# Performance work log

Hardware: AMD Instinct MI355X
Metric: run time of the kernel (lower is better)

The kernel has to match this reference:

```python
import jax, jax.numpy as jnp
import numpy as np


def _bitrev_indices(N):
    # bit-reversal permutation, vectorized in numpy (static, N known at trace time)
    bits = int(np.log2(N))
    idx = np.arange(N, dtype=np.int64)
    rev = np.zeros(N, dtype=np.int64)
    for _ in range(bits):
        rev = (rev << 1) | (idx & 1)
        idx >>= 1
    return jnp.asarray(rev)


def setup_inputs() -> dict:
    key = jax.random.key(0)
    k1, k2 = jax.random.split(key)
    B, N = 2048, 4096
    return {
        "x_re": jax.random.normal(k1, (B, N), dtype=jnp.float32),
        "x_im": jax.random.normal(k2, (B, N), dtype=jnp.float32),
    }


def reference(x_re, x_im):
    # Radix-2 decimation-in-time Cooley-Tukey FFT, faithful to PythonFFT.forward
    N = x_re.shape[-1]
    batch = x_re.shape[:-1]
    num_stages = int(np.log2(N))

    # twiddle table W_N^k = exp(-2*pi*i*k/N) (matches compute_twiddle_table)
    k = jnp.arange(N, dtype=jnp.float32)
    angles = (-2.0 * np.pi) * k / N
    W_re_tab = jnp.cos(angles)
    W_im_tab = jnp.sin(angles)

    br = _bitrev_indices(N)
    y_re = x_re[..., br]
    y_im = x_im[..., br]

    # loop over log2(N) stages (small fixed loop); each stage is fully vectorized
    for stage in range(num_stages):
        stride = 1 << stage
        group = stride << 1
        # twiddle index for butterfly position j in a group: j * (N // group) % N
        tw_idx = (jnp.arange(stride) * (N // group)) % N
        w_re = W_re_tab[tw_idx]  # [stride]
        w_im = W_im_tab[tw_idx]  # [stride]

        yr = y_re.reshape(*batch, N // group, 2, stride)
        yi = y_im.reshape(*batch, N // group, 2, stride)
        a_re, b_re = yr[..., 0, :], yr[..., 1, :]
        a_im, b_im = yi[..., 0, :], yi[..., 1, :]

        wb_re = w_re * b_re - w_im * b_im
        wb_im = w_re * b_im + w_im * b_re

        y_re = jnp.stack([a_re + wb_re, a_re - wb_re], axis=-2).reshape(*batch, N)
        y_im = jnp.stack([a_im + wb_im, a_im - wb_im], axis=-2).reshape(*batch, N)

    return (y_re, y_im)
```

## Files before the change

### kernel.cpp

```cpp
#include <hip/hip_runtime.h>
#include <math.h>

#define FFT_N   4096
#define LOGN    12
#define THREADS 512
#define NEG2PI_N (-1.5339807878856412e-3f)

__device__ __forceinline__ int SW2(int i) { return i ^ ((i >> 5) & 31); }

__device__ __forceinline__ float2 cmul(float2 a, float2 b) {
    return make_float2(a.x * b.x - a.y * b.y, a.x * b.y + a.y * b.x);
}

__device__ __forceinline__ void bfly(float2& a, float2& b, float2 w) {
    float tr = w.x * b.x - w.y * b.y;
    float ti = w.x * b.y + w.y * b.x;
    b = make_float2(a.x - tr, a.y - ti);
    a = make_float2(a.x + tr, a.y + ti);
}

template<int ST, bool WRITE>
__device__ __forceinline__ void radix8_stage(float2* __restrict__ sd, int t, float2* v)
{
    const int s    = 1 << ST;
    const int lo   = t & (s - 1);
    const int base = ((t >> ST) << (ST + 3)) | lo;

    int addr[8];
    #pragma unroll
    for (int k = 0; k < 8; ++k) addr[k] = SW2(base + k * s);
    #pragma unroll
    for (int k = 0; k < 8; ++k) v[k] = sd[addr[k]];

    float ang = (float)(lo << (9 - ST)) * NEG2PI_N;
    float sn, cs;
    __sincosf(ang, &sn, &cs);
    const float2 wc0 = make_float2(cs, sn);
    const float2 wb0 = cmul(wc0, wc0);
    const float2 wa  = cmul(wb0, wb0);

    bfly(v[0], v[1], wa); bfly(v[2], v[3], wa);
    bfly(v[4], v[5], wa); bfly(v[6], v[7], wa);

    const float2 wb1 = make_float2(wb0.y, -wb0.x);
    bfly(v[0], v[2], wb0); bfly(v[1], v[3], wb1);
    bfly(v[4], v[6], wb0); bfly(v[5], v[7], wb1);

    const float RH = 0.70710678118654752f;
    const float2 wc1 = cmul(wc0, make_float2(RH, -RH));
    const float2 wc2 = make_float2(wc0.y, -wc0.x);
    const float2 wc3 = cmul(wc0, make_float2(-RH, -RH));
    bfly(v[0], v[4], wc0); bfly(v[1], v[5], wc1);
    bfly(v[2], v[6], wc2); bfly(v[3], v[7], wc3);

    if (WRITE) {
        #pragma unroll
        for (int k = 0; k < 8; ++k) sd[addr[k]] = v[k];
    }
}

__global__ __launch_bounds__(THREADS)
void fft4096_r8(const float* __restrict__ xre, const float* __restrict__ xim,
                float* __restrict__ yre, float* __restrict__ yim)
{
    __shared__ float2 sd[FFT_N];
    const int t = threadIdx.x;
    const size_t off = (size_t)blockIdx.x * FFT_N;

    const float4* xr4 = (const float4*)(xre + off);
    const float4* xi4 = (const float4*)(xim + off);
    float4 r0 = xr4[t];
    float4 r1 = xr4[t + THREADS];
    float4 m0 = xi4[t];
    float4 m1 = xi4[t + THREADS];

    const int rb = (int)(__brev((unsigned)t) >> 23) << 1;
    sd[SW2(rb + (0 << 10))]     = make_float2(r0.x, m0.x);
    sd[SW2(rb + (2 << 10))]     = make_float2(r0.y, m0.y);
    sd[SW2(rb + (1 << 10))]     = make_float2(r0.z, m0.z);
    sd[SW2(rb + (3 << 10))]     = make_float2(r0.w, m0.w);
    sd[SW2(rb + 1)]             = make_float2(r1.x, m1.x);
    sd[SW2(rb + 1 + (2 << 10))] = make_float2(r1.y, m1.y);
    sd[SW2(rb + 1 + (1 << 10))] = make_float2(r1.z, m1.z);
    sd[SW2(rb + 1 + (3 << 10))] = make_float2(r1.w, m1.w);
    __syncthreads();

    float2 v[8];
    radix8_stage<0, true>(sd, t, v);  __syncthreads();
    radix8_stage<3, true>(sd, t, v);  __syncthreads();
    radix8_stage<6, true>(sd, t, v);  __syncthreads();
    radix8_stage<9, false>(sd, t, v);

    float* yr = yre + off;
    float* yi = yim + off;
    #pragma unroll
    for (int k = 0; k < 8; ++k) {
        yr[t + (k << 9)] = v[k].x;
        yi[t + (k << 9)] = v[k].y;
    }
}

extern "C" void kernel_launch(void* const* d_in, const int* in_sizes, int n_in,
                              void* d_out, int out_size, void* d_ws, size_t ws_size,
                              hipStream_t stream) {
    const float* xre = (const float*)d_in[0];
    const float* xim = (const float*)d_in[1];
    const int total = in_sizes[0];
    const int rows  = total / FFT_N;
    float* yre = (float*)d_out;
    float* yim = yre + total;
    fft4096_r8<<<dim3(rows), dim3(THREADS), 0, stream>>>(xre, xim, yre, yim);
}
```

Before: 27.32 us.

## Restructure FFT as 64x64 four-step with wave-shuffle inner radix-64

Replaces the four radix-8 shared-memory stages with a 64x64 four-step decomposition. Each 64-point sub-FFT is done as a per-thread DFT8 followed by cross-lane xor-shuffle butterflies. The result is one shared-memory transpose with an XOR swizzle and a single barrier instead of three. Global loads become strided scalar loads rather than float4, and each shuffle stage adds cross-lane traffic and twiddle sincos work in exchange for fewer LDS round trips and syncs.

Result: slower. 32.70 us (+19.7%).

```diff
diff --git a/kernel.cpp b/kernel.cpp
--- a/kernel.cpp
+++ b/kernel.cpp
@@ -2,101 +2,147 @@
 #include <math.h>
 
 #define FFT_N   4096
-#define LOGN    12
 #define THREADS 512
-#define NEG2PI_N (-1.5339807878856412e-3f)
-
-__device__ __forceinline__ int SW2(int i) { return i ^ ((i >> 5) & 31); }
+#define RH 0.70710678118654752f
+#define NEG2PI_64   (-9.81747704246810387e-2f)
+#define NEG2PI_4096 (-1.53398078788564123e-3f)
 
 __device__ __forceinline__ float2 cmul(float2 a, float2 b) {
     return make_float2(a.x * b.x - a.y * b.y, a.x * b.y + a.y * b.x);
 }
-
-__device__ __forceinline__ void bfly(float2& a, float2& b, float2 w) {
-    float tr = w.x * b.x - w.y * b.y;
-    float ti = w.x * b.y + w.y * b.x;
-    b = make_float2(a.x - tr, a.y - ti);
-    a = make_float2(a.x + tr, a.y + ti);
+__device__ __forceinline__ void bfly1(float2& a, float2& b) {
+    float2 t = b;
+    b = make_float2(a.x - t.x, a.y - t.y);
+    a = make_float2(a.x + t.x, a.y + t.y);
+}
+__device__ __forceinline__ void bflyNi(float2& a, float2& b) {
+    float2 t = make_float2(b.y, -b.x);
+    b = make_float2(a.x - t.x, a.y - t.y);
+    a = make_float2(a.x + t.x, a.y + t.y);
+}
+__device__ __forceinline__ void bflyW(float2& a, float2& b, float2 w) {
+    float2 t = cmul(w, b);
+    b = make_float2(a.x - t.x, a.y - t.y);
+    a = make_float2(a.x + t.x, a.y + t.y);
 }
 
-template<int ST, bool WRITE>
-__device__ __forceinline__ void radix8_stage(float2* __restrict__ sd, int t, float2* v)
-{
-    const int s    = 1 << ST;
-    const int lo   = t & (s - 1);
-    const int base = ((t >> ST) << (ST + 3)) | lo;
+__device__ __forceinline__ void dft8(float2 v[8]) {
+    float2 n0 = v[0], n1 = v[4], n2 = v[2], n3 = v[6];
+    float2 n4 = v[1], n5 = v[5], n6 = v[3], n7 = v[7];
+    bfly1(n0, n1); bfly1(n2, n3); bfly1(n4, n5); bfly1(n6, n7);
+    bfly1(n0, n2); bflyNi(n1, n3); bfly1(n4, n6); bflyNi(n5, n7);
+    const float2 w81 = make_float2(RH, -RH), w83 = make_float2(-RH, -RH);
+    bfly1(n0, n4); bflyW(n1, n5, w81); bflyNi(n2, n6); bflyW(n3, n7, w83);
+    v[0] = n0; v[1] = n1; v[2] = n2; v[3] = n3;
+    v[4] = n4; v[5] = n5; v[6] = n6; v[7] = n7;
+}
 
-    int addr[8];
+__device__ __forceinline__ float2 shflx(float2 v, int mask) {
+    return make_float2(__shfl_xor(v.x, mask, 64), __shfl_xor(v.y, mask, 64));
+}
+
+__device__ __forceinline__ void lane_dif8(float2 v[8], float s1, float2 w1,
+                                          float s2, float2 w2, float s3) {
     #pragma unroll
-    for (int k = 0; k < 8; ++k) addr[k] = SW2(base + k * s);
+    for (int r = 0; r < 8; ++r) {
+        float2 p = shflx(v[r], 32);
+        float2 t = make_float2(fmaf(s1, v[r].x, p.x), fmaf(s1, v[r].y, p.y));
+        v[r] = cmul(t, w1);
+    }
     #pragma unroll
-    for (int k = 0; k < 8; ++k) v[k] = sd[addr[k]];
-
-    float ang = (float)(lo << (9 - ST)) * NEG2PI_N;
-    float sn, cs;
-    __sincosf(ang, &sn, &cs);
-    const float2 wc0 = make_float2(cs, sn);
-    const float2 wb0 = cmul(wc0, wc0);
-    const float2 wa  = cmul(wb0, wb0);
-
-    bfly(v[0], v[1], wa); bfly(v[2], v[3], wa);
-    bfly(v[4], v[5], wa); bfly(v[6], v[7], wa);
-
-    const float2 wb1 = make_float2(wb0.y, -wb0.x);
-    bfly(v[0], v[2], wb0); bfly(v[1], v[3], wb1);
-    bfly(v[4], v[6], wb0); bfly(v[5], v[7], wb1);
-
-    const float RH = 0.70710678118654752f;
-    const float2 wc1 = cmul(wc0, make_float2(RH, -RH));
-    const float2 wc2 = make_float2(wc0.y, -wc0.x);
-    const float2 wc3 = cmul(wc0, make_float2(-RH, -RH));
-    bfly(v[0], v[4], wc0); bfly(v[1], v[5], wc1);
-    bfly(v[2], v[6], wc2); bfly(v[3], v[7], wc3);
-
-    if (WRITE) {
-        #pragma unroll
-        for (int k = 0; k < 8; ++k) sd[addr[k]] = v[k];
+    for (int r = 0; r < 8; ++r) {
+        float2 p = shflx(v[r], 16);
+        float2 t = make_float2(fmaf(s2, v[r].x, p.x), fmaf(s2, v[r].y, p.y));
+        v[r] = cmul(t, w2);
+    }
+    #pragma unroll
+    for (int r = 0; r < 8; ++r) {
+        float2 p = shflx(v[r], 8);
+        v[r] = make_float2(fmaf(s3, v[r].x, p.x), fmaf(s3, v[r].y, p.y));
     }
 }
 
 __global__ __launch_bounds__(THREADS)
-void fft4096_r8(const float* __restrict__ xre, const float* __restrict__ xim,
-                float* __restrict__ yre, float* __restrict__ yim)
+void fft4096_6464(const float* __restrict__ xre, const float* __restrict__ xim,
+                  float* __restrict__ yre, float* __restrict__ yim)
 {
     __shared__ float2 sd[FFT_N];
-    const int t = threadIdx.x;
+
+    const int tid = threadIdx.x;
+    const int w  = tid >> 6;
+    const int l  = tid & 63;
+    const int lh = l >> 3;
+    const int ll = l & 7;
+    const int rb = ((lh & 1) << 2) | (lh & 2) | ((lh >> 2) & 1);
     const size_t off = (size_t)blockIdx.x * FFT_N;
 
-    const float4* xr4 = (const float4*)(xre + off);
-    const float4* xi4 = (const float4*)(xim + off);
-    float4 r0 = xr4[t];
-    float4 r1 = xr4[t + THREADS];
-    float4 m0 = xi4[t];
-    float4 m1 = xi4[t + THREADS];
+    const int c = lh & 3;
+    const float wx = (c == 0) ? 1.f : (c == 1) ? RH : (c == 2) ? 0.f : -RH;
+    const float wy = (c == 0) ? 0.f : (c == 2) ? -1.f : -RH;
+    const float2 w1 = (lh & 4) ? make_float2(wx, wy) : make_float2(1.f, 0.f);
+    const float2 w2 = (lh & 2) ? ((lh & 1) ? make_float2(0.f, -1.f)
+                                           : make_float2(1.f, 0.f))
+                               : make_float2(1.f, 0.f);
+    const float s1 = (lh & 4) ? -1.f : 1.f;
+    const float s2 = (lh & 2) ? -1.f : 1.f;
+    const float s3 = (lh & 1) ? -1.f : 1.f;
 
-    const int rb = (int)(__brev((unsigned)t) >> 23) << 1;
-    sd[SW2(rb + (0 << 10))]     = make_float2(r0.x, m0.x);
-    sd[SW2(rb + (2 << 10))]     = make_float2(r0.y, m0.y);
-    sd[SW2(rb + (1 << 10))]     = make_float2(r0.z, m0.z);
-    sd[SW2(rb + (3 << 10))]     = make_float2(r0.w, m0.w);
-    sd[SW2(rb + 1)]             = make_float2(r1.x, m1.x);
-    sd[SW2(rb + 1 + (2 << 10))] = make_float2(r1.y, m1.y);
-    sd[SW2(rb + 1 + (1 << 10))] = make_float2(r1.z, m1.z);
-    sd[SW2(rb + 1 + (3 << 10))] = make_float2(r1.w, m1.w);
+    const int n1v  = 8 * w + ll;
+    const int base = n1v + 64 * lh;
+    const float* xr = xre + off;
+    const float* xi = xim + off;
+    float2 v[8];
+    #pragma unroll
+    for (int r = 0; r < 8; ++r) {
+        v[r].x = xr[base + 512 * r];
+        v[r].y = xi[base + 512 * r];
+    }
+
+    dft8(v);
+    #pragma unroll
+    for (int r = 1; r < 8; ++r) {
+        float sn, cs;
+        __sincosf((float)(lh * r) * NEG2PI_64, &sn, &cs);
+        v[r] = cmul(v[r], make_float2(cs, sn));
+    }
+    lane_dif8(v, s1, w1, s2, w2, s3);
+
+    #pragma unroll
+    for (int r = 0; r < 8; ++r) {
+        const int k1 = r + (rb << 3);
+        float sn, cs;
+        __sincosf((float)(n1v * k1) * NEG2PI_4096, &sn, &cs);
+        float2 t = cmul(v[r], make_float2(cs, sn));
+        const int g = 9 * ((k1 & 7) ^ (k1 >> 3));
+        sd[(k1 << 6) | (n1v ^ g)] = t;
+    }
     __syncthreads();
+    {
+        const int k1m = 8 * w + ll;
+        const int gm  = 9 * ((k1m & 7) ^ (k1m >> 3));
+        #pragma unroll
+        for (int r = 0; r < 8; ++r) {
+            const int n1 = lh + 8 * r;
+            v[r] = sd[(k1m << 6) | (n1 ^ gm)];
+        }
+    }
 
-    float2 v[8];
-    radix8_stage<0, true>(sd, t, v);  __syncthreads();
-    radix8_stage<3, true>(sd, t, v);  __syncthreads();
-    radix8_stage<6, true>(sd, t, v);  __syncthreads();
-    radix8_stage<9, false>(sd, t, v);
+    dft8(v);
+    #pragma unroll
+    for (int r = 1; r < 8; ++r) {
+        float sn, cs;
+        __sincosf((float)(lh * r) * NEG2PI_64, &sn, &cs);
+        v[r] = cmul(v[r], make_float2(cs, sn));
+    }
+    lane_dif8(v, s1, w1, s2, w2, s3);
 
     float* yr = yre + off;
     float* yi = yim + off;
+    const int sb = 8 * w + ll + 512 * rb;
     #pragma unroll
-    for (int k = 0; k < 8; ++k) {
-        yr[t + (k << 9)] = v[k].x;
-        yi[t + (k << 9)] = v[k].y;
+    for (int r = 0; r < 8; ++r) {
+        yr[sb + 64 * r] = v[r].x;
+        yi[sb + 64 * r] = v[r].y;
     }
 }
 
@@ -109,5 +155,5 @@
     const int rows  = total / FFT_N;
     float* yre = (float*)d_out;
     float* yim = yre + total;
-    fft4096_r8<<<dim3(rows), dim3(THREADS), 0, stream>>>(xre, xim, yre, yim);
+    fft4096_6464<<<dim3(rows), dim3(THREADS), 0, stream>>>(xre, xim, yre, yim);
 }
```

## Replace radix-8 DIT FFT with three-pass radix-16 four-step FFT

Applied to the files above, without the earlier changes.

Restructures the 4096-point FFT from four radix-8 passes at 512 threads into three radix-16 passes at 256 threads. Each thread loads 16 strided points directly from global memory, with no bit-reversal scatter, and does the first DFT16 in registers. Twiddles are generated by sincos plus recurrence multiplication, and data goes through shared memory only twice, using XOR-swizzled indices to limit bank conflicts. This cuts shared-memory traffic and barriers but raises register pressure with 16 complex values per thread. The recurrence twiddles may also accumulate slightly more rounding error.

New measurement: 26.80 us. Within noise of the previous version (-1.9%).

```diff
diff --git a/kernel.cpp b/kernel.cpp
--- a/kernel.cpp
+++ b/kernel.cpp
@@ -2,101 +2,123 @@
 #include <math.h>
 
 #define FFT_N   4096
-#define LOGN    12
-#define THREADS 512
-#define NEG2PI_N (-1.5339807878856412e-3f)
+#define THREADS 256
+#define RH 0.70710678118654752f
+#define C16 0.92387953251128676f
+#define S16 0.38268343236508977f
+#define NEG2PI_256  (-2.45436926061702597e-2f)
+#define NEG2PI_4096 (-1.53398078788564123e-3f)
 
-__device__ __forceinline__ int SW2(int i) { return i ^ ((i >> 5) & 31); }
+#define POS(k) ((((k) & 3) << 2) | ((k) >> 2))
 
 __device__ __forceinline__ float2 cmul(float2 a, float2 b) {
     return make_float2(a.x * b.x - a.y * b.y, a.x * b.y + a.y * b.x);
 }
 
-__device__ __forceinline__ void bfly(float2& a, float2& b, float2 w) {
-    float tr = w.x * b.x - w.y * b.y;
-    float ti = w.x * b.y + w.y * b.x;
-    b = make_float2(a.x - tr, a.y - ti);
-    a = make_float2(a.x + tr, a.y + ti);
+__device__ __forceinline__ void dft4(float2& a, float2& b, float2& c, float2& d) {
+    float2 t0 = make_float2(a.x + c.x, a.y + c.y);
+    float2 t1 = make_float2(a.x - c.x, a.y - c.y);
+    float2 t2 = make_float2(b.x + d.x, b.y + d.y);
+    float2 t3 = make_float2(b.y - d.y, d.x - b.x);
+    a = make_float2(t0.x + t2.x, t0.y + t2.y);
+    b = make_float2(t1.x + t3.x, t1.y + t3.y);
+    c = make_float2(t0.x - t2.x, t0.y - t2.y);
+    d = make_float2(t1.x - t3.x, t1.y - t3.y);
 }
 
-template<int ST, bool WRITE>
-__device__ __forceinline__ void radix8_stage(float2* __restrict__ sd, int t, float2* v)
-{
-    const int s    = 1 << ST;
-    const int lo   = t & (s - 1);
-    const int base = ((t >> ST) << (ST + 3)) | lo;
+template<int E>
+__device__ __forceinline__ float2 mw16(float2 z) {
+    if constexpr (E == 0) return z;
+    else if constexpr (E == 4) return make_float2(z.y, -z.x);
+    else if constexpr (E == 2) return make_float2(RH * (z.x + z.y), RH * (z.y - z.x));
+    else if constexpr (E == 6) return make_float2(RH * (z.y - z.x), -RH * (z.x + z.y));
+    else if constexpr (E == 1) return cmul(z, make_float2(C16, -S16));
+    else if constexpr (E == 3) return cmul(z, make_float2(S16, -C16));
+    else           return cmul(z, make_float2(-C16, S16));
+}
 
-    int addr[8];
-    #pragma unroll
-    for (int k = 0; k < 8; ++k) addr[k] = SW2(base + k * s);
-    #pragma unroll
-    for (int k = 0; k < 8; ++k) v[k] = sd[addr[k]];
-
-    float ang = (float)(lo << (9 - ST)) * NEG2PI_N;
-    float sn, cs;
-    __sincosf(ang, &sn, &cs);
-    const float2 wc0 = make_float2(cs, sn);
-    const float2 wb0 = cmul(wc0, wc0);
-    const float2 wa  = cmul(wb0, wb0);
-
-    bfly(v[0], v[1], wa); bfly(v[2], v[3], wa);
-    bfly(v[4], v[5], wa); bfly(v[6], v[7], wa);
-
-    const float2 wb1 = make_float2(wb0.y, -wb0.x);
-    bfly(v[0], v[2], wb0); bfly(v[1], v[3], wb1);
-    bfly(v[4], v[6], wb0); bfly(v[5], v[7], wb1);
-
-    const float RH = 0.70710678118654752f;
-    const float2 wc1 = cmul(wc0, make_float2(RH, -RH));
-    const float2 wc2 = make_float2(wc0.y, -wc0.x);
-    const float2 wc3 = cmul(wc0, make_float2(-RH, -RH));
-    bfly(v[0], v[4], wc0); bfly(v[1], v[5], wc1);
-    bfly(v[2], v[6], wc2); bfly(v[3], v[7], wc3);
-
-    if (WRITE) {
-        #pragma unroll
-        for (int k = 0; k < 8; ++k) sd[addr[k]] = v[k];
-    }
+__device__ __forceinline__ void dft16(float2 (&v)[16]) {
+    dft4(v[0], v[4], v[8],  v[12]);
+    dft4(v[1], v[5], v[9],  v[13]);
+    dft4(v[2], v[6], v[10], v[14]);
+    dft4(v[3], v[7], v[11], v[15]);
+    v[5]  = mw16<1>(v[5]);   v[9]  = mw16<2>(v[9]);   v[13] = mw16<3>(v[13]);
+    v[6]  = mw16<2>(v[6]);   v[10] = mw16<4>(v[10]);  v[14] = mw16<6>(v[14]);
+    v[7]  = mw16<3>(v[7]);   v[11] = mw16<6>(v[11]);  v[15] = mw16<9>(v[15]);
+    dft4(v[0],  v[1],  v[2],  v[3]);
+    dft4(v[4],  v[5],  v[6],  v[7]);
+    dft4(v[8],  v[9],  v[10], v[11]);
+    dft4(v[12], v[13], v[14], v[15]);
 }
 
 __global__ __launch_bounds__(THREADS)
-void fft4096_r8(const float* __restrict__ xre, const float* __restrict__ xim,
-                float* __restrict__ yre, float* __restrict__ yim)
+void fft4096_r16(const float* __restrict__ xre, const float* __restrict__ xim,
+                 float* __restrict__ yre, float* __restrict__ yim)
 {
     __shared__ float2 sd[FFT_N];
-    const int t = threadIdx.x;
+
+    const int t  = threadIdx.x;
+    const int lo = t & 15;
+    const int hi = t >> 4;
     const size_t off = (size_t)blockIdx.x * FFT_N;
+    const float* xr = xre + off;
+    const float* xi = xim + off;
 
-    const float4* xr4 = (const float4*)(xre + off);
-    const float4* xi4 = (const float4*)(xim + off);
-    float4 r0 = xr4[t];
-    float4 r1 = xr4[t + THREADS];
-    float4 m0 = xi4[t];
-    float4 m1 = xi4[t + THREADS];
+    float2 v[16];
+    #pragma unroll
+    for (int n3 = 0; n3 < 16; ++n3) {
+        v[n3].x = xr[t + (n3 << 8)];
+        v[n3].y = xi[t + (n3 << 8)];
+    }
+    dft16(v);
 
-    const int rb = (int)(__brev((unsigned)t) >> 23) << 1;
-    sd[SW2(rb + (0 << 10))]     = make_float2(r0.x, m0.x);
-    sd[SW2(rb + (2 << 10))]     = make_float2(r0.y, m0.y);
-    sd[SW2(rb + (1 << 10))]     = make_float2(r0.z, m0.z);
-    sd[SW2(rb + (3 << 10))]     = make_float2(r0.w, m0.w);
-    sd[SW2(rb + 1)]             = make_float2(r1.x, m1.x);
-    sd[SW2(rb + 1 + (2 << 10))] = make_float2(r1.y, m1.y);
-    sd[SW2(rb + 1 + (1 << 10))] = make_float2(r1.z, m1.z);
-    sd[SW2(rb + 1 + (3 << 10))] = make_float2(r1.w, m1.w);
+    {
+        float sn, cs;
+        __sincosf((float)hi * NEG2PI_256, &sn, &cs);
+        const float2 base = make_float2(cs, sn);
+        float2 P = base;
+        sd[t] = v[POS(0)];
+        #pragma unroll
+        for (int k3 = 1; k3 < 16; ++k3) {
+            sd[t + (k3 << 8)] = cmul(v[POS(k3)], P);
+            P = cmul(P, base);
+        }
+    }
     __syncthreads();
 
-    float2 v[8];
-    radix8_stage<0, true>(sd, t, v);  __syncthreads();
-    radix8_stage<3, true>(sd, t, v);  __syncthreads();
-    radix8_stage<6, true>(sd, t, v);  __syncthreads();
-    radix8_stage<9, false>(sd, t, v);
+    #pragma unroll
+    for (int n2 = 0; n2 < 16; ++n2)
+        v[n2] = sd[lo + (n2 << 4) + (hi << 8)];
+    __syncthreads();
 
+    dft16(v);
+
+    {
+        float sn, cs;
+        __sincosf((float)(lo * hi) * NEG2PI_4096, &sn, &cs);
+        float2 P = make_float2(cs, sn);
+        __sincosf((float)lo * NEG2PI_256, &sn, &cs);
+        const float2 base = make_float2(cs, sn);
+        const int wb = (hi ^ lo) + (lo << 8);
+        #pragma unroll
+        for (int k2 = 0; k2 < 16; ++k2) {
+            sd[wb + (k2 << 4)] = cmul(v[POS(k2)], P);
+            P = cmul(P, base);
+        }
+    }
+    __syncthreads();
+
+    #pragma unroll
+    for (int m = 0; m < 16; ++m)
+        v[m] = sd[(lo ^ m) + (hi << 4) + (m << 8)];
+
+    dft16(v);
     float* yr = yre + off;
     float* yi = yim + off;
     #pragma unroll
-    for (int k = 0; k < 8; ++k) {
-        yr[t + (k << 9)] = v[k].x;
-        yi[t + (k << 9)] = v[k].y;
+    for (int k1 = 0; k1 < 16; ++k1) {
+        yr[t + (k1 << 8)] = v[POS(k1)].x;
+        yi[t + (k1 << 8)] = v[POS(k1)].y;
     }
 }
 
@@ -109,5 +131,5 @@
     const int rows  = total / FFT_N;
     float* yre = (float*)d_out;
     float* yim = yre + total;
-    fft4096_r8<<<dim3(rows), dim3(THREADS), 0, stream>>>(xre, xim, yre, yim);
+    fft4096_r16<<<dim3(rows), dim3(THREADS), 0, stream>>>(xre, xim, yre, yim);
 }
```
